# Kernel tuning notes

Hardware: AMD Instinct MI355X
Metric: run time of the kernel (lower is better)

Reference implementation:

```python
import jax, jax.numpy as jnp
import numpy as np

B, I, O, G = 262144, 3, 64, 128


def setup_inputs() -> dict:
    key = jax.random.key(0)
    kx, kc = jax.random.split(key)
    x = jax.random.uniform(kx, (1, B, I), dtype=jnp.float32)  # coords in [0,1)
    coeffs = jax.random.normal(kc, (2, O, I, G), dtype=jnp.float32) / (
        np.float32(np.sqrt(I) * np.sqrt(G))
    )
    bias = jnp.zeros((1, O), dtype=jnp.float32)
    return {"x": x, "coeffs": coeffs, "bias": bias}


def reference(x, coeffs, bias):
    # x: (1, B, I); coeffs: (2, O, I, G); bias: (1, O)
    b, i = x.shape[1], x.shape[2]
    two, o, _, g = coeffs.shape
    k = jnp.arange(1, g + 1, dtype=x.dtype)          # (G,)
    kx = x.reshape(b, i, 1) * k                      # (B, I, G)
    cosf = jnp.cos(kx).reshape(b, i * g)             # (B, I*G)
    sinf = jnp.sin(kx).reshape(b, i * g)             # (B, I*G)
    w = coeffs.reshape(2, o, i * g)                  # (2, O, I*G)
    # sum over (input_dim, gridsize) fused as one GEMM per trig branch
    out = cosf @ w[0].T + sinf @ w[1].T + bias       # (B, O)
    return out
```

## Files before the change

### kernel.cpp

```cpp
#include <hip/hip_runtime.h>
#include <hip/hip_bf16.h>

typedef __attribute__((ext_vector_type(8))) short short8;
typedef __attribute__((ext_vector_type(4))) float f32x4;
typedef __attribute__((ext_vector_type(2))) float f32x2;
typedef __attribute__((ext_vector_type(4))) unsigned int u32x4;

#define NROWS   262144
#define ODIM    64
#define NBLOCKS 256
#define TPB     1024
#define INV2PI  0.15915494309189535f

__device__ __forceinline__ float cos2pi(float f){ float r; asm("v_cos_f32 %0, %1" : "=v"(r) : "v"(f)); return r; }
__device__ __forceinline__ float sin2pi(float f){ float r; asm("v_sin_f32 %0, %1" : "=v"(r) : "v"(f)); return r; }
__device__ __forceinline__ f32x2 pk_mul(f32x2 a, f32x2 b){
    f32x2 d; asm("v_pk_mul_f32 %0, %1, %2" : "=v"(d) : "v"(a), "v"(b)); return d; }
__device__ __forceinline__ f32x2 pk_fma(f32x2 a, f32x2 b, f32x2 c){
    f32x2 d; asm("v_pk_fma_f32 %0, %1, %2, %3" : "=v"(d) : "v"(a), "v"(b), "v"(c)); return d; }
__device__ __forceinline__ f32x2 pk_fms(f32x2 a, f32x2 b, f32x2 c){
    f32x2 d; asm("v_pk_fma_f32 %0, %1, %2, %3 neg_lo:[0,0,1] neg_hi:[0,0,1]"
                 : "=v"(d) : "v"(a), "v"(b), "v"(c)); return d; }
__device__ __forceinline__ unsigned pkbf(float lo, float hi){
    unsigned r; asm("v_cvt_pk_bf16_f32 %0, %1, %2" : "=v"(r) : "v"(lo), "v"(hi)); return r; }
__device__ __forceinline__ short8 as_s8(u32x4 v){ union{u32x4 u; short8 s;} x; x.u = v; return x.s; }
__device__ __forceinline__ short bf16_of(float f){
    union { __hip_bfloat16 h; short s; } u; u.h = __float2bfloat16(f); return u.s; }

extern "C" __global__ void __launch_bounds__(TPB, 4)
fourier_mfma(const float* __restrict__ x,
             const float* __restrict__ coeffs,
             const float* __restrict__ bias,
             float* __restrict__ out)
{
    __shared__ short8 Wlds[24 * 4 * 64];

    const int tid = threadIdx.x;

    for (int fl = tid; fl < 24*4*64; fl += TPB) {
        const int ks = fl >> 8;
        const int nt = (fl >> 6) & 3;
        const int ln = fl & 63;
        const int o  = nt*16 + (ln & 15);
        const int kg = ln >> 4;
        union { short8 v; short s[8]; } fr;
        #pragma unroll
        for (int h = 0; h < 2; ++h) {
            const int kb  = ks*32 + h*16;
            const int br  = (kb >= 384) ? 1 : 0;
            const int rem = kb - br*384;
            const int ii  = rem >> 7;
            const int g0  = (rem & 127) + kg*4;
            const float* wp = coeffs + (((br*ODIM + o)*3 + ii) << 7) + g0;
            #pragma unroll
            for (int j = 0; j < 4; ++j) fr.s[h*4 + j] = bf16_of(wp[j]);
        }
        Wlds[fl] = fr.v;
    }
    __syncthreads();

    const int lane = tid & 63;
    const int wid  = tid >> 6;
    const int mrow = lane & 15;
    const int kgrp = lane >> 4;
    const float hs = (float)(4*kgrp + 1);

    float bcol[4];
    #pragma unroll
    for (int nt = 0; nt < 4; ++nt) bcol[nt] = bias[nt*16 + mrow];

    const int unit = blockIdx.x * 16 + wid;
    const int base = unit * 64;

    #pragma unroll 1
    for (int rg = 0; rg < 2; ++rg) {
        const int rowA = base + (rg*2 + 0)*16 + mrow;
        const int rowB = base + (rg*2 + 1)*16 + mrow;

        f32x2 xr[3];
        #pragma unroll
        for (int i = 0; i < 3; ++i)
            xr[i] = (f32x2){ x[rowA*3 + i] * INV2PI, x[rowB*3 + i] * INV2PI };

        f32x4 acc[2][4];
        #pragma unroll
        for (int rr = 0; rr < 2; ++rr)
            #pragma unroll
            for (int nt = 0; nt < 4; ++nt)
                acc[rr][nt] = (f32x4){0.f, 0.f, 0.f, 0.f};

        f32x2 cvp, svp, c16p, s16p, stc, sts;

        #pragma unroll 1
        for (int kk = 0; kk < 12; ++kk) {
            short8 bfr[8];
            #pragma unroll
            for (int nt = 0; nt < 4; ++nt) {
                bfr[nt]     = Wlds[(kk*4 + nt)*64 + lane];
                bfr[4 + nt] = Wlds[((kk + 12)*4 + nt)*64 + lane];
            }

            if ((kk & 3) == 0) {
                const int i = kk >> 2;
                const f32x2 a = xr[i];
                cvp = (f32x2){ cos2pi(a.x), cos2pi(a.y) };
                svp = (f32x2){ sin2pi(a.x), sin2pi(a.y) };
                f32x2 t = (f32x2){ 16.f*a.x, 16.f*a.y };
                t.x -= floorf(t.x); t.y -= floorf(t.y);
                c16p = (f32x2){ cos2pi(t.x), cos2pi(t.y) };
                s16p = (f32x2){ sin2pi(t.x), sin2pi(t.y) };
                f32x2 u = (f32x2){ hs*a.x, hs*a.y };
                u.x -= floorf(u.x); u.y -= floorf(u.y);
                stc = (f32x2){ cos2pi(u.x), cos2pi(u.y) };
                sts = (f32x2){ sin2pi(u.x), sin2pi(u.y) };
            }

            u32x4 FCA, FCB, FSA, FSB;
            {
                f32x2 c0 = stc, s0 = sts;
                f32x2 c1 = pk_fms(c0, cvp, pk_mul(s0, svp));
                f32x2 s1 = pk_fma(s0, cvp, pk_mul(c0, svp));
                FCA.x = pkbf(c0.x, c1.x);  FCB.x = pkbf(c0.y, c1.y);
                FSA.x = pkbf(s0.x, s1.x);  FSB.x = pkbf(s0.y, s1.y);
                f32x2 c2 = pk_fms(c1, cvp, pk_mul(s1, svp));
                f32x2 s2 = pk_fma(s1, cvp, pk_mul(c1, svp));
                f32x2 c3 = pk_fms(c2, cvp, pk_mul(s2, svp));
                f32x2 s3 = pk_fma(s2, cvp, pk_mul(c2, svp));
                FCA.y = pkbf(c2.x, c3.x);  FCB.y = pkbf(c2.y, c3.y);
                FSA.y = pkbf(s2.x, s3.x);  FSB.y = pkbf(s2.y, s3.y);
                f32x2 nc = pk_fms(stc, c16p, pk_mul(sts, s16p));
                f32x2 ns = pk_fma(sts, c16p, pk_mul(stc, s16p));
                stc = nc; sts = ns;
                c0 = stc; s0 = sts;
                c1 = pk_fms(c0, cvp, pk_mul(s0, svp));
                s1 = pk_fma(s0, cvp, pk_mul(c0, svp));
                FCA.z = pkbf(c0.x, c1.x);  FCB.z = pkbf(c0.y, c1.y);
                FSA.z = pkbf(s0.x, s1.x);  FSB.z = pkbf(s0.y, s1.y);
                c2 = pk_fms(c1, cvp, pk_mul(s1, svp));
                s2 = pk_fma(s1, cvp, pk_mul(c1, svp));
                c3 = pk_fms(c2, cvp, pk_mul(s2, svp));
                s3 = pk_fma(s2, cvp, pk_mul(c2, svp));
                FCA.w = pkbf(c2.x, c3.x);  FCB.w = pkbf(c2.y, c3.y);
                FSA.w = pkbf(s2.x, s3.x);  FSB.w = pkbf(s2.y, s3.y);
                nc = pk_fms(stc, c16p, pk_mul(sts, s16p));
                ns = pk_fma(sts, c16p, pk_mul(stc, s16p));
                stc = nc; sts = ns;
            }

            const short8 fAc = as_s8(FCA);
            const short8 fBc = as_s8(FCB);
            const short8 fAs = as_s8(FSA);
            const short8 fBs = as_s8(FSB);

            #pragma unroll
            for (int nt = 0; nt < 4; ++nt)
                acc[0][nt] = __builtin_amdgcn_mfma_f32_16x16x32_bf16(fAc, bfr[nt], acc[0][nt], 0, 0, 0);
            #pragma unroll
            for (int nt = 0; nt < 4; ++nt)
                acc[1][nt] = __builtin_amdgcn_mfma_f32_16x16x32_bf16(fBc, bfr[nt], acc[1][nt], 0, 0, 0);
            #pragma unroll
            for (int nt = 0; nt < 4; ++nt)
                acc[0][nt] = __builtin_amdgcn_mfma_f32_16x16x32_bf16(fAs, bfr[4+nt], acc[0][nt], 0, 0, 0);
            #pragma unroll
            for (int nt = 0; nt < 4; ++nt)
                acc[1][nt] = __builtin_amdgcn_mfma_f32_16x16x32_bf16(fBs, bfr[4+nt], acc[1][nt], 0, 0, 0);
        }

        #pragma unroll
        for (int rr = 0; rr < 2; ++rr) {
            const int row0 = base + (rg*2 + rr)*16 + kgrp*4;
            #pragma unroll
            for (int nt = 0; nt < 4; ++nt) {
                #pragma unroll
                for (int q = 0; q < 4; ++q) {
                    out[(row0 + q)*ODIM + nt*16 + mrow] = acc[rr][nt][q] + bcol[nt];
                }
            }
        }
    }
}

extern "C" void kernel_launch(void* const* d_in, const int* in_sizes, int n_in,
                              void* d_out, int out_size, void* d_ws, size_t ws_size,
                              hipStream_t stream) {
    const float* x      = (const float*)d_in[0];
    const float* coeffs = (const float*)d_in[1];
    const float* bias   = (const float*)d_in[2];
    float* out = (float*)d_out;
    (void)in_sizes; (void)n_in; (void)out_size; (void)d_ws; (void)ws_size;
    hipLaunchKernelGGL(fourier_mfma, dim3(NBLOCKS), dim3(TPB), 0, stream, x, coeffs, bias, out);
}
```

Measured before the change: 42.37 us.

## Split K across waves with register-resident weights and LDS reduction

Replaces the LDS-staged weight fragments with a K-split: each of four waves holds a quarter of the bf16 weight fragments in registers for its K slice, so weights are no longer reread from LDS every K step. Partial accumulators for each 64-row unit go to shared memory and are summed across the four K waves, with bias added and written out in row-major, coalesced order. This drops the per-step LDS weight loads and makes output stores coalesced, but adds two block barriers and an LDS reduction per unit. It also changes the launch shape to 512 blocks of 512 threads and raises register pressure.

```diff
diff --git a/kernel.cpp b/kernel.cpp
--- a/kernel.cpp
+++ b/kernel.cpp
@@ -8,8 +8,9 @@
 
 #define NROWS   262144
 #define ODIM    64
-#define NBLOCKS 256
-#define TPB     1024
+#define NBLOCKS 512
+#define TPB     512
+#define UPB     8
 #define INV2PI  0.15915494309189535f
 
 __device__ __forceinline__ float cos2pi(float f){ float r; asm("v_cos_f32 %0, %1" : "=v"(r) : "v"(f)); return r; }
@@ -27,55 +28,55 @@
 __device__ __forceinline__ short bf16_of(float f){
     union { __hip_bfloat16 h; short s; } u; u.h = __float2bfloat16(f); return u.s; }
 
-extern "C" __global__ void __launch_bounds__(TPB, 4)
-fourier_mfma(const float* __restrict__ x,
-             const float* __restrict__ coeffs,
-             const float* __restrict__ bias,
-             float* __restrict__ out)
+extern "C" __global__ void __launch_bounds__(TPB, 2)
+fourier_ksplit(const float* __restrict__ x,
+               const float* __restrict__ coeffs,
+               const float* __restrict__ bias,
+               float* __restrict__ out)
 {
-    __shared__ short8 Wlds[24 * 4 * 64];
-
-    const int tid = threadIdx.x;
-
-    for (int fl = tid; fl < 24*4*64; fl += TPB) {
-        const int ks = fl >> 8;
-        const int nt = (fl >> 6) & 3;
-        const int ln = fl & 63;
-        const int o  = nt*16 + (ln & 15);
-        const int kg = ln >> 4;
-        union { short8 v; short s[8]; } fr;
-        #pragma unroll
-        for (int h = 0; h < 2; ++h) {
-            const int kb  = ks*32 + h*16;
-            const int br  = (kb >= 384) ? 1 : 0;
-            const int rem = kb - br*384;
-            const int ii  = rem >> 7;
-            const int g0  = (rem & 127) + kg*4;
-            const float* wp = coeffs + (((br*ODIM + o)*3 + ii) << 7) + g0;
-            #pragma unroll
-            for (int j = 0; j < 4; ++j) fr.s[h*4 + j] = bf16_of(wp[j]);
-        }
-        Wlds[fl] = fr.v;
-    }
-    __syncthreads();
-
+    __shared__ float Plds[8][32*64];
+
+    const int tid  = threadIdx.x;
     const int lane = tid & 63;
     const int wid  = tid >> 6;
+    const int rh   = wid >> 2;
+    const int kw   = wid & 3;
     const int mrow = lane & 15;
     const int kgrp = lane >> 4;
+
+    short8 Breg[3][2][4];
+    #pragma unroll
+    for (int c = 0; c < 3; ++c) {
+        #pragma unroll
+        for (int br = 0; br < 2; ++br) {
+            #pragma unroll
+            for (int nt = 0; nt < 4; ++nt) {
+                const int ks = 3*kw + c;
+                const int o  = nt*16 + mrow;
+                union { short8 v; short s[8]; } fr;
+                #pragma unroll
+                for (int h = 0; h < 2; ++h) {
+                    const int rem = ks*32 + h*16;
+                    const int ii  = rem >> 7;
+                    const int g0  = (rem & 127) + kgrp*4;
+                    const float* wp = coeffs + (((br*ODIM + o)*3 + ii) << 7) + g0;
+                    #pragma unroll
+                    for (int j = 0; j < 4; ++j) fr.s[h*4 + j] = bf16_of(wp[j]);
+                }
+                Breg[c][br][nt] = fr.v;
+            }
+        }
+    }
+
     const float hs = (float)(4*kgrp + 1);
-
-    float bcol[4];
-    #pragma unroll
-    for (int nt = 0; nt < 4; ++nt) bcol[nt] = bias[nt*16 + mrow];
-
-    const int unit = blockIdx.x * 16 + wid;
-    const int base = unit * 64;
+    const float bv = bias[lane];
 
     #pragma unroll 1
-    for (int rg = 0; rg < 2; ++rg) {
-        const int rowA = base + (rg*2 + 0)*16 + mrow;
-        const int rowB = base + (rg*2 + 1)*16 + mrow;
+    for (int uu = 0; uu < UPB; ++uu) {
+        const int unit  = blockIdx.x * UPB + uu;
+        const int rbase = unit*64 + rh*32;
+        const int rowA  = rbase + mrow;
+        const int rowB  = rbase + 16 + mrow;
 
         f32x2 xr[3];
         #pragma unroll
@@ -84,32 +85,28 @@
 
         f32x4 acc[2][4];
         #pragma unroll
-        for (int rr = 0; rr < 2; ++rr)
-            #pragma unroll
-            for (int nt = 0; nt < 4; ++nt)
-                acc[rr][nt] = (f32x4){0.f, 0.f, 0.f, 0.f};
+        for (int rt = 0; rt < 2; ++rt)
+            #pragma unroll
+            for (int nt = 0; nt < 4; ++nt)
+                acc[rt][nt] = (f32x4){0.f, 0.f, 0.f, 0.f};
 
         f32x2 cvp, svp, c16p, s16p, stc, sts;
 
-        #pragma unroll 1
-        for (int kk = 0; kk < 12; ++kk) {
-            short8 bfr[8];
-            #pragma unroll
-            for (int nt = 0; nt < 4; ++nt) {
-                bfr[nt]     = Wlds[(kk*4 + nt)*64 + lane];
-                bfr[4 + nt] = Wlds[((kk + 12)*4 + nt)*64 + lane];
-            }
-
-            if ((kk & 3) == 0) {
-                const int i = kk >> 2;
-                const f32x2 a = xr[i];
+        #pragma unroll
+        for (int c = 0; c < 3; ++c) {
+            const int p = 3*kw + c;
+            if (c == 0 || (p & 3) == 0) {
+                const int ii = p >> 2;
+                const float moff = (float)(32 * (p & 3));
+                const f32x2 a = xr[ii];
                 cvp = (f32x2){ cos2pi(a.x), cos2pi(a.y) };
                 svp = (f32x2){ sin2pi(a.x), sin2pi(a.y) };
                 f32x2 t = (f32x2){ 16.f*a.x, 16.f*a.y };
                 t.x -= floorf(t.x); t.y -= floorf(t.y);
                 c16p = (f32x2){ cos2pi(t.x), cos2pi(t.y) };
                 s16p = (f32x2){ sin2pi(t.x), sin2pi(t.y) };
-                f32x2 u = (f32x2){ hs*a.x, hs*a.y };
+                const float hm = hs + moff;
+                f32x2 u = (f32x2){ hm*a.x, hm*a.y };
                 u.x -= floorf(u.x); u.y -= floorf(u.y);
                 stc = (f32x2){ cos2pi(u.x), cos2pi(u.y) };
                 sts = (f32x2){ sin2pi(u.x), sin2pi(u.y) };
@@ -154,28 +151,42 @@
 
             #pragma unroll
             for (int nt = 0; nt < 4; ++nt)
-                acc[0][nt] = __builtin_amdgcn_mfma_f32_16x16x32_bf16(fAc, bfr[nt], acc[0][nt], 0, 0, 0);
-            #pragma unroll
-            for (int nt = 0; nt < 4; ++nt)
-                acc[1][nt] = __builtin_amdgcn_mfma_f32_16x16x32_bf16(fBc, bfr[nt], acc[1][nt], 0, 0, 0);
-            #pragma unroll
-            for (int nt = 0; nt < 4; ++nt)
-                acc[0][nt] = __builtin_amdgcn_mfma_f32_16x16x32_bf16(fAs, bfr[4+nt], acc[0][nt], 0, 0, 0);
-            #pragma unroll
-            for (int nt = 0; nt < 4; ++nt)
-                acc[1][nt] = __builtin_amdgcn_mfma_f32_16x16x32_bf16(fBs, bfr[4+nt], acc[1][nt], 0, 0, 0);
-        }
-
-        #pragma unroll
-        for (int rr = 0; rr < 2; ++rr) {
-            const int row0 = base + (rg*2 + rr)*16 + kgrp*4;
-            #pragma unroll
-            for (int nt = 0; nt < 4; ++nt) {
+                acc[0][nt] = __builtin_amdgcn_mfma_f32_16x16x32_bf16(fAc, Breg[c][0][nt], acc[0][nt], 0, 0, 0);
+            #pragma unroll
+            for (int nt = 0; nt < 4; ++nt)
+                acc[1][nt] = __builtin_amdgcn_mfma_f32_16x16x32_bf16(fBc, Breg[c][0][nt], acc[1][nt], 0, 0, 0);
+            #pragma unroll
+            for (int nt = 0; nt < 4; ++nt)
+                acc[0][nt] = __builtin_amdgcn_mfma_f32_16x16x32_bf16(fAs, Breg[c][1][nt], acc[0][nt], 0, 0, 0);
+            #pragma unroll
+            for (int nt = 0; nt < 4; ++nt)
+                acc[1][nt] = __builtin_amdgcn_mfma_f32_16x16x32_bf16(fBs, Breg[c][1][nt], acc[1][nt], 0, 0, 0);
+        }
+
+        __syncthreads();
+
+        {
+            const int slot = rh*4 + kw;
+            #pragma unroll
+            for (int rt = 0; rt < 2; ++rt)
                 #pragma unroll
-                for (int q = 0; q < 4; ++q) {
-                    out[(row0 + q)*ODIM + nt*16 + mrow] = acc[rr][nt][q] + bcol[nt];
-                }
-            }
+                for (int nt = 0; nt < 4; ++nt)
+                    #pragma unroll
+                    for (int q = 0; q < 4; ++q)
+                        Plds[slot][((rt*4 + nt)*4 + q)*64 + lane] = acc[rt][nt][q];
+        }
+
+        __syncthreads();
+
+        #pragma unroll
+        for (int rr = 0; rr < 8; ++rr) {
+            const int r     = wid*8 + rr;
+            const int lane2 = (((r & 15) >> 2) << 4) | (lane & 15);
+            const int reg   = (((r >> 4) & 1)*4 + (lane >> 4))*4 + (r & 3);
+            const int sb    = (r >> 5)*4;
+            const float s = Plds[sb+0][reg*64 + lane2] + Plds[sb+1][reg*64 + lane2]
+                          + Plds[sb+2][reg*64 + lane2] + Plds[sb+3][reg*64 + lane2];
+            out[(unit*64 + r)*ODIM + lane] = s + bv;
         }
     }
 }
@@ -188,5 +199,5 @@
     const float* bias   = (const float*)d_in[2];
     float* out = (float*)d_out;
     (void)in_sizes; (void)n_in; (void)out_size; (void)d_ws; (void)ws_size;
-    hipLaunchKernelGGL(fourier_mfma, dim3(NBLOCKS), dim3(TPB), 0, stream, x, coeffs, bias, out);
+    hipLaunchKernelGGL(fourier_ksplit, dim3(NBLOCKS), dim3(TPB), 0, stream, x, coeffs, bias, out);
 }
```

New measurement: 69.73 us. +64.6%, slower.
